# Kernel tuning notes

Hardware: AMD Instinct MI355X
Metric: run time of the kernel (lower is better)

## Reference

```python
import jax, jax.numpy as jnp
import numpy as np

B, C, N, D = 8192, 1000, 2, 512
EPS = 0.1  # epsilon init arg


def setup_inputs() -> dict:
    key = jax.random.key(0)
    kx, kc, kr = jax.random.split(key, 3)
    x = jax.random.normal(kx, (B, D), dtype=jnp.float32)
    centroids = jax.random.uniform(kc, (C, N, D), minval=-1.0, maxval=1.0, dtype=jnp.float32)
    rej_raw = jax.random.uniform(kr, (C * N, D), minval=-1.0, maxval=1.0, dtype=jnp.float32)
    # replicate the __init__ rescaling of the (frozen) rejective centroids
    cmax = jnp.max(jnp.linalg.norm(centroids, axis=-1))
    rej = 2.0 * cmax * rej_raw / (jnp.linalg.norm(rej_raw, axis=-1, keepdims=True) + 1e-16)
    return {"x": x, "centroids": centroids, "rejective_centroids": rej, "return_dists": 1}


def reference(x, centroids, rejective_centroids, return_dists):
    b, d = x.shape
    c, n, _ = centroids.shape
    t = c * n
    # centroid_norm is updated via .data in torch -> detached
    cnorm = jax.lax.stop_gradient(jnp.max(jnp.linalg.norm(centroids, axis=-1)))
    cf = (centroids / (cnorm + 1e-16)).reshape(t, d)  # [T, D] normalized centroids
    # pairwise L2 distances via the expansion identity (no [B,T,D] intermediate)
    x2 = jnp.sum(x * x, axis=-1)          # [B]
    c2 = jnp.sum(cf * cf, axis=-1)        # [T]
    d2 = jnp.maximum(x2[:, None] + c2[None, :] - 2.0 * (x @ cf.T), 0.0)
    dist = jnp.sqrt(d2)                   # [B, T]
    min_dist_class = jnp.min(dist.reshape(b, c, n), axis=2)  # [B, C]
    y = -min_dist_class
    if return_dists:
        idx = jnp.argmin(dist, axis=1)                 # [B]
        closest = cf[idx]                              # [B, D] gathered closest centroid
        r = rejective_centroids                        # [T, D]
        r2 = jnp.sum(r * r, axis=-1)                   # [T]
        xr = x @ r.T                                   # [B, T]
        cr = closest @ r.T                             # [B, T]
        cx = jnp.sum(closest * x, axis=-1)             # [B]
        cl2 = jnp.sum(closest * closest, axis=-1)      # [B]
        # w = closest - r ; b_off = -w . (closest + r)/2 = -0.5(|c|^2 - |r|^2)
        num = jnp.abs(cx[:, None] - xr - 0.5 * (cl2[:, None] - r2[None, :]))
        den = jnp.sqrt(jnp.maximum(cl2[:, None] + r2[None, :] - 2.0 * cr, 0.0)) + 1e-9
        rej_hd = jnp.min(num / den, axis=-1)           # [B]
        return jnp.concatenate([y, rej_hd[:, None]], axis=1)
    min_d = jnp.min(min_dist_class, axis=1)
    removed = jnp.where(min_dist_class == min_d[:, None], jnp.inf, min_dist_class)
    second = jnp.min(removed, axis=1)
    y_bot = -(1.0 - EPS) / (1.0 + EPS) * second
    accept = min_d - EPS * (min_d + second)
    soft = jax.nn.sigmoid(accept)  # ac_temp == 1
    return jnp.concatenate([y, y_bot[:, None], soft[:, None]], axis=1)
```

## Files before the change

### kernel.cpp

```cpp
#include <hip/hip_runtime.h>
#include <math.h>
#include <stdint.h>

#define NB   8192
#define NCLS 1000
#define NT   2000
#define ND   512
#define OUTW 1001

#define OFF_NORM2C 0
#define OFF_R2     2048
#define OFF_X2     4096
#define OFF_SCAL   12288
#define OFF_IDX    12352
#define OFF_CX     20544
#define OFF_CL2    28736

#define NOFF_MIND  36928
#define NOFF_REJP  823360

#define OFF8_MIND  36928
#define OFF8_MINT  102464
#define OFF8_MDOT  168000
#define OFF8_REJP  233536

#define PACKX_B  (8ull<<20)
#define PACKC_B  (24ull<<20)
#define PACKR_B  (28ull<<20)
#define PACKT_B  (32ull<<20)
#define WS_NEED  (48ull<<20)

typedef __attribute__((ext_vector_type(8))) short bf16x8;
typedef __attribute__((ext_vector_type(4))) float f32x4;

__global__ __launch_bounds__(64) void rownorm_kernel(
    const float* __restrict__ cen, const float* __restrict__ rej,
    const float* __restrict__ x, float* __restrict__ ws)
{
    int row = blockIdx.x;
    int lane = threadIdx.x;
    const float* src;
    int dstoff;
    if (row < NT)        { src = cen + (size_t)row * ND;          dstoff = OFF_NORM2C + row; }
    else if (row < 2*NT) { src = rej + (size_t)(row - NT) * ND;   dstoff = OFF_R2 + (row - NT); }
    else                 { src = x   + (size_t)(row - 2*NT) * ND; dstoff = OFF_X2 + (row - 2*NT); }
    float s = 0.f;
#pragma unroll
    for (int k = 0; k < ND / 64; ++k) { float v = src[lane + k * 64]; s += v * v; }
#pragma unroll
    for (int off = 32; off > 0; off >>= 1) s += __shfl_down(s, off);
    if (lane == 0) ws[dstoff] = s;
}

__global__ __launch_bounds__(256) void maxnorm_kernel(float* __restrict__ ws)
{
    __shared__ float sm[256];
    int tid = threadIdx.x;
    float m = 0.f;
    for (int i = tid; i < NT; i += 256) m = fmaxf(m, ws[OFF_NORM2C + i]);
    sm[tid] = m;
    __syncthreads();
    for (int s = 128; s > 0; s >>= 1) {
        if (tid < s) sm[tid] = fmaxf(sm[tid], sm[tid + s]);
        __syncthreads();
    }
    if (tid == 0) {
        float cnorm = sqrtf(sm[0]);
        float inv = 1.f / (cnorm + 1e-16f);
        ws[OFF_SCAL + 0] = cnorm;
        ws[OFF_SCAL + 1] = inv;
        ws[OFF_SCAL + 2] = inv * inv;
    }
}

__device__ __forceinline__ ushort bf16rn(float f){
    uint32_t u = __float_as_uint(f);
    return (ushort)((u + 0x7fffu + ((u >> 16) & 1u)) >> 16);
}

__global__ __launch_bounds__(256) void pack_kernel(const float* __restrict__ src,
    unsigned char* __restrict__ dst, int validRows)
{
    int tid = threadIdx.x;
    int lane = tid & 63;
    int W = blockIdx.x * 4 + (tid >> 6);
    int s  = W >> 4;
    int ks = W & 15;
    int row = s * 16 + (lane & 15);
    int k   = ks * 32 + (lane >> 4) * 8;
    float v[8];
    if (row < validRows) {
        float4 a = *(const float4*)&src[(size_t)row * ND + k];
        float4 b = *(const float4*)&src[(size_t)row * ND + k + 4];
        v[0]=a.x; v[1]=a.y; v[2]=a.z; v[3]=a.w;
        v[4]=b.x; v[5]=b.y; v[6]=b.z; v[7]=b.w;
    } else {
#pragma unroll
        for (int j = 0; j < 8; ++j) v[j] = 0.f;
    }
    union { ushort h[8]; uint4 q; } H, L;
#pragma unroll
    for (int j = 0; j < 8; ++j) {
        ushort hb = bf16rn(v[j]);
        float hf = __uint_as_float(((uint32_t)hb) << 16);
        H.h[j] = hb;
        L.h[j] = bf16rn(v[j] - hf);
    }
    size_t base = ((size_t)(((s >> 3) * 16 + ks) * 16 + (s & 7) * 2)) * 1024;
    *(uint4*)(dst + base + lane * 16)        = H.q;
    *(uint4*)(dst + base + 1024 + lane * 16) = L.q;
}

typedef __attribute__((address_space(3))) unsigned int lds_u32;
typedef const __attribute__((address_space(1))) unsigned int glb_u32;
__device__ __forceinline__ void gload_lds16(const unsigned char* g, unsigned char* l) {
    __builtin_amdgcn_global_load_lds((glb_u32*)g, (lds_u32*)l, 16, 0, 0);
}

template<bool BLO>
__device__ __forceinline__ void stage256(
    const unsigned char* __restrict__ aP2, const unsigned char* __restrict__ bP2,
    int ks, unsigned char* lbuf, int wave, int lane)
{
    if (wave < 4) {
#pragma unroll
        for (int j = 0; j < 8; ++j) {
            int gc = wave * 8 + j;
            gload_lds16(aP2 + (gc >> 4) * 262144 + ks * 16384 + (gc & 15) * 1024 + lane * 16,
                        lbuf + gc * 1024);
        }
    } else {
        if constexpr (BLO) {
#pragma unroll
            for (int j = 0; j < 8; ++j) {
                int gc = (wave - 4) * 8 + j;
                gload_lds16(bP2 + (gc >> 4) * 262144 + ks * 16384 + (gc & 15) * 1024 + lane * 16,
                            lbuf + 32768 + gc * 1024);
            }
        } else {
#pragma unroll
            for (int j = 0; j < 4; ++j) {
                int gc = (wave - 4) * 4 + j;
                gload_lds16(bP2 + (gc >> 3) * 262144 + ks * 16384 + ((gc & 7) * 2) * 1024 + lane * 16,
                            lbuf + 32768 + gc * 1024);
            }
        }
    }
}

#define PASS8(av, bv) do { _Pragma("unroll") \
    for (int qi = 0; qi < 4; ++qi) \
        _Pragma("unroll") \
        for (int ri = 0; ri < 8; ++ri) \
            acc[ri][qi] = __builtin_amdgcn_mfma_f32_16x16x32_bf16( \
                av[ri], bv[qi], acc[ri][qi], 0, 0, 0); \
    } while (0)

template<bool BLO>
__device__ __forceinline__ void compute_step256(
    const unsigned char* __restrict__ cbuf, int lane, int wr, int wc, f32x4 acc[8][4])
{
    const unsigned char* aB = cbuf + wr * 16384 + lane * 16;
    const unsigned char* bB = BLO
        ? cbuf + 32768 + (wc >> 1) * 16384 + ((wc & 1) * 4) * 2048 + lane * 16
        : cbuf + 32768 + (wc >> 1) * 8192  + ((wc & 1) * 4) * 1024 + lane * 16;
    bf16x8 bh[4];
#pragma unroll
    for (int qi = 0; qi < 4; ++qi) bh[qi] = *(const bf16x8*)(bB + qi * (BLO ? 2048 : 1024));
    if constexpr (BLO) {
        bf16x8 bl[4];
#pragma unroll
        for (int qi = 0; qi < 4; ++qi) bl[qi] = *(const bf16x8*)(bB + qi * 2048 + 1024);
        {
            bf16x8 a[8];
#pragma unroll
            for (int ri = 0; ri < 8; ++ri) a[ri] = *(const bf16x8*)(aB + ri * 2048);
            PASS8(a, bh);
            PASS8(a, bl);
        }
        {
            bf16x8 a[8];
#pragma unroll
            for (int ri = 0; ri < 8; ++ri) a[ri] = *(const bf16x8*)(aB + ri * 2048 + 1024);
            PASS8(a, bh);
        }
    } else {
        {
            bf16x8 a[8];
#pragma unroll
            for (int ri = 0; ri < 8; ++ri) a[ri] = *(const bf16x8*)(aB + ri * 2048);
            PASS8(a, bh);
        }
        {
            bf16x8 a[8];
#pragma unroll
            for (int ri = 0; ri < 8; ++ri) a[ri] = *(const bf16x8*)(aB + ri * 2048 + 1024);
            PASS8(a, bh);
        }
    }
}

#define SCHED_FENCE __builtin_amdgcn_sched_barrier(0)

template<bool BLO>
__device__ __forceinline__ void mfma_core256_pipe(
    const unsigned char* __restrict__ aP2, const unsigned char* __restrict__ bP2,
    unsigned char* lds, int lane, int wave, int wr, int wc, f32x4 acc[8][4])
{
    constexpr int BUF = BLO ? 65536 : 49152;
    stage256<BLO>(aP2, bP2, 0, lds, wave, lane);
    for (int ks = 0; ks < 16; ++ks) {
        unsigned char* cbuf = lds + (ks & 1) * BUF;
        unsigned char* nbuf = lds + ((ks + 1) & 1) * BUF;
        if (ks < 15) {
            stage256<BLO>(aP2, bP2, ks + 1, nbuf, wave, lane);
            SCHED_FENCE;
            if (BLO || wave < 4) asm volatile("s_waitcnt vmcnt(8)" ::: "memory");
            else                 asm volatile("s_waitcnt vmcnt(4)" ::: "memory");
            SCHED_FENCE;
        } else {
            SCHED_FENCE;
            asm volatile("s_waitcnt vmcnt(0)" ::: "memory");
            SCHED_FENCE;
        }
        __builtin_amdgcn_s_barrier();
        __builtin_amdgcn_s_setprio(1);
        compute_step256<BLO>(cbuf, lane, wr, wc, acc);
        __builtin_amdgcn_s_setprio(0);
        __builtin_amdgcn_s_barrier();
    }
}

__global__ __launch_bounds__(512) void dist_mfma_kernel(
    const unsigned char* __restrict__ xpack, const unsigned char* __restrict__ cpack,
    float* __restrict__ out, float* __restrict__ ws)
{
    __shared__ unsigned char lds[2 * 65536];
    int tid = threadIdx.x, lane = tid & 63, wave = tid >> 6;
    int wr = wave >> 2, wc = wave & 3;
    int xb = blockIdx.x, yb = blockIdx.y;
    int b0 = xb * 256, t0base = yb * 256;
    f32x4 acc[8][4];
#pragma unroll
    for (int i = 0; i < 8; ++i)
#pragma unroll
        for (int q = 0; q < 4; ++q) acc[i][q] = (f32x4){0.f, 0.f, 0.f, 0.f};
    mfma_core256_pipe<true>(xpack + (size_t)xb * 524288, cpack + (size_t)yb * 524288,
                            lds, lane, wave, wr, wc, acc);

    float inv  = ws[OFF_SCAL + 1];
    float inv2 = ws[OFF_SCAL + 2];
    int rq = lane >> 4, cidx = lane & 15;
    int seg = yb * 4 + wc;
    float c2q[4]; int tq[4];
#pragma unroll
    for (int qi = 0; qi < 4; ++qi) {
        int t = t0base + wc * 64 + qi * 16 + cidx;
        tq[qi] = t;
        c2q[qi] = (t < NT) ? ws[OFF_NORM2C + t] * inv2 : 0.f;
    }
    unsigned long long* keys = (unsigned long long*)(ws + NOFF_MIND);

#pragma unroll
    for (int ri = 0; ri < 8; ++ri) {
#pragma unroll
        for (int reg = 0; reg < 4; ++reg) {
            int row = b0 + wr * 128 + ri * 16 + rq * 4 + reg;
            float x2 = ws[OFF_X2 + row];
            unsigned long long best = ~0ull;
#pragma unroll
            for (int qi = 0; qi < 4; ++qi) {
                float dsc = acc[ri][qi][reg] * inv;
                float dd = sqrtf(fmaxf(x2 + c2q[qi] - 2.f * dsc, 0.f));
                float dn = __shfl_xor(dd, 1);
                int t = tq[qi];
                if ((t < NT) && ((cidx & 1) == 0))
                    out[(size_t)row * OUTW + (t >> 1)] = -fminf(dd, dn);
                if (t < NT) {
                    unsigned long long key =
                        ((unsigned long long)__float_as_uint(dd) << 32) | (unsigned)t;
                    best = best < key ? best : key;
                }
            }
#pragma unroll
            for (int off = 1; off < 16; off <<= 1) {
                unsigned long long o = __shfl_xor(best, off);
                best = best < o ? best : o;
            }
            if (cidx == 0) keys[(size_t)row * 32 + seg] = best;
        }
    }
}

__global__ __launch_bounds__(256) void combine32_kernel(float* __restrict__ ws)
{
    int b = blockIdx.x * 256 + threadIdx.x;
    const unsigned long long* keys = (const unsigned long long*)(ws + NOFF_MIND);
    unsigned long long best = keys[(size_t)b * 32];
#pragma unroll
    for (int s = 1; s < 32; ++s) {
        unsigned long long k = keys[(size_t)b * 32 + s];
        best = best < k ? best : k;
    }
    int bt = (int)(best & 0xffffffffull);
    float dd = __uint_as_float((unsigned)(best >> 32));
    float c2 = ws[OFF_NORM2C + bt] * ws[OFF_SCAL + 2];
    float x2 = ws[OFF_X2 + b];
    ((int*)ws)[OFF_IDX + b] = bt;
    ws[OFF_CX + b] = 0.5f * (x2 + c2 - dd * dd);
    ws[OFF_CL2 + b] = c2;
}

#define LOADA(buf, ks_) do { _Pragma("unroll") \
    for (int i = 0; i < 4; ++i) { \
        buf[i]     = *(const bf16x8*)(aB + (ks_) * 16384 + i * 2048); \
        buf[4 + i] = *(const bf16x8*)(aB + (ks_) * 16384 + i * 2048 + 1024); \
    } } while (0)
#define LOADB2(buf, ks_) do { _Pragma("unroll") \
    for (int i = 0; i < 4; ++i) { \
        buf[i] = *(const bf16x8*)(bB + (ks_) * 16384 + i * 2048); \
    } } while (0)
#define PASS(av, bv, AOFF, BOFF) do { _Pragma("unroll") \
    for (int qi = 0; qi < 4; ++qi) \
        _Pragma("unroll") \
        for (int ri = 0; ri < 4; ++ri) \
            acc[ri][qi] = __builtin_amdgcn_mfma_f32_16x16x32_bf16( \
                av[(AOFF) + ri], bv[(BOFF) + qi], acc[ri][qi], 0, 0, 0); \
    } while (0)
#define COMPUTE2(av, bv) do { PASS(av, bv, 0, 0); PASS(av, bv, 4, 0); } while (0)

__device__ __forceinline__ void mfma_core_db2(
    const unsigned char* __restrict__ aP, const unsigned char* __restrict__ bP,
    int lane, int wr, int wc, f32x4 acc[4][4])
{
    const unsigned char* aB = aP + wr * 8192 + lane * 16;
    const unsigned char* bB = bP + wc * 8192 + lane * 16;
    bf16x8 a0[8], a1[8], b0[4], b1[4];
    LOADA(a0, 0); LOADB2(b0, 0);
    for (int ks = 0; ks < 16; ks += 2) {
        LOADA(a1, ks + 1); LOADB2(b1, ks + 1);
        COMPUTE2(a0, b0);
        if (ks + 2 < 16) { LOADA(a0, ks + 2); LOADB2(b0, ks + 2); }
        COMPUTE2(a1, b1);
    }
}

__global__ __launch_bounds__(256, 2) void table_mfma_kernel(
    const unsigned char* __restrict__ cpack, const unsigned char* __restrict__ rpack,
    float* __restrict__ table, const float* __restrict__ ws)
{
    int tid = threadIdx.x, lane = tid & 63, wave = tid >> 6;
    int wr = wave >> 1, wc = wave & 1;
    int c0 = blockIdx.x * 128, t0base = blockIdx.y * 128;
    f32x4 acc[4][4];
#pragma unroll
    for (int i = 0; i < 4; ++i)
#pragma unroll
        for (int q = 0; q < 4; ++q) acc[i][q] = (f32x4){0.f, 0.f, 0.f, 0.f};
    mfma_core_db2(cpack + (size_t)blockIdx.x * 262144, rpack + (size_t)blockIdx.y * 262144,
                  lane, wr, wc, acc);

    float inv  = ws[OFF_SCAL + 1];
    float inv2 = ws[OFF_SCAL + 2];
    int rq = lane >> 4, cidx = lane & 15;
    float r2q[4]; int tq[4];
#pragma unroll
    for (int qi = 0; qi < 4; ++qi) {
        int t = t0base + wc * 64 + qi * 16 + cidx;
        tq[qi] = t;
        r2q[qi] = (t < NT) ? ws[OFF_R2 + t] : 0.f;
    }
#pragma unroll
    for (int ri = 0; ri < 4; ++ri) {
#pragma unroll
        for (int reg = 0; reg < 4; ++reg) {
            int c = c0 + wr * 64 + ri * 16 + rq * 4 + reg;
            if (c < NT) {
                float cl2c = ws[OFF_NORM2C + c] * inv2;
#pragma unroll
                for (int qi = 0; qi < 4; ++qi) {
                    int t = tq[qi];
                    if (t < NT) {
                        float cfr = acc[ri][qi][reg] * inv;
                        float den = sqrtf(fmaxf(cl2c + r2q[qi] - 2.f * cfr, 0.f)) + 1e-9f;
                        table[(size_t)c * 2048 + t] = 1.f / den;
                    }
                }
            }
        }
    }
}

__global__ __launch_bounds__(512) void xr_mfma_kernel(
    const unsigned char* __restrict__ xpack, const unsigned char* __restrict__ rpack,
    const float* __restrict__ table, float* __restrict__ ws)
{
    __shared__ unsigned char lds[2 * 49152];
    int tid = threadIdx.x, lane = tid & 63, wave = tid >> 6;
    int wr = wave >> 2, wc = wave & 3;
    int xb = blockIdx.x, yb = blockIdx.y;
    int b0 = xb * 256, t0base = yb * 256;
    f32x4 acc[8][4];
#pragma unroll
    for (int i = 0; i < 8; ++i)
#pragma unroll
        for (int q = 0; q < 4; ++q) acc[i][q] = (f32x4){0.f, 0.f, 0.f, 0.f};
    mfma_core256_pipe<false>(xpack + (size_t)xb * 524288, rpack + (size_t)yb * 524288,
                             lds, lane, wave, wr, wc, acc);

    int rq = lane >> 4, cidx = lane & 15;
    int seg = yb * 4 + wc;
    float r2q[4]; int tq[4];
#pragma unroll
    for (int qi = 0; qi < 4; ++qi) {
        int t = t0base + wc * 64 + qi * 16 + cidx;
        tq[qi] = t;
        r2q[qi] = (t < NT) ? ws[OFF_R2 + t] : 0.f;
    }
#pragma unroll
    for (int ri = 0; ri < 8; ++ri) {
#pragma unroll
        for (int reg = 0; reg < 4; ++reg) {
            int row = b0 + wr * 128 + ri * 16 + rq * 4 + reg;
            int idx = ((const int*)ws)[OFF_IDX + row];
            float cx  = ws[OFF_CX + row];
            float cl2 = ws[OFF_CL2 + row];
            const float* trow = table + (size_t)idx * 2048;
            float mv = INFINITY;
#pragma unroll
            for (int qi = 0; qi < 4; ++qi) {
                int t = tq[qi];
                if (t < NT) {
                    float num = fabsf(cx - acc[ri][qi][reg] - 0.5f * (cl2 - r2q[qi]));
                    mv = fminf(mv, num * trow[t]);
                }
            }
#pragma unroll
            for (int off = 1; off < 16; off <<= 1) mv = fminf(mv, __shfl_xor(mv, off));
            if (cidx == 0) ws[NOFF_REJP + (size_t)row * 32 + seg] = mv;
        }
    }
}

__global__ __launch_bounds__(256) void rejcombine32_kernel(
    const float* __restrict__ ws, float* __restrict__ out)
{
    int b = blockIdx.x * 256 + threadIdx.x;
    float bd = ws[NOFF_REJP + (size_t)b * 32];
#pragma unroll
    for (int s = 1; s < 32; ++s) bd = fminf(bd, ws[NOFF_REJP + (size_t)b * 32 + s]);
    out[(size_t)b * OUTW + NCLS] = bd;
}

#define BK   32
#define LDST 68

__global__ __launch_bounds__(256) void dist_kernel(
    const float* __restrict__ x, const float* __restrict__ cen,
    float* __restrict__ out, float* __restrict__ ws)
{
    __shared__ float Xs[BK][LDST];
    __shared__ float Cs[BK][LDST];
    __shared__ float red_d[64][17];
    __shared__ int   red_t[64][17];
    __shared__ float red_x[64][17];

    int tid = threadIdx.x;
    int tx = tid & 15, ty = tid >> 4;
    int b0 = blockIdx.x * 64;
    int tseg0 = blockIdx.y * 256;
    int tseg1 = min(tseg0 + 256, NT);

    float inv  = ws[OFF_SCAL + 1];
    float inv2 = ws[OFF_SCAL + 2];
    float x2v[4];
#pragma unroll
    for (int i = 0; i < 4; ++i) x2v[i] = ws[OFF_X2 + b0 + ty * 4 + i];

    int lr = tid >> 2;
    int lc = (tid & 3) * 8;

    float mind[4], mdot[4];
    int mint[4];
#pragma unroll
    for (int i = 0; i < 4; ++i) { mind[i] = INFINITY; mint[i] = 0x7fffffff; mdot[i] = 0.f; }

    for (int t0 = tseg0; t0 < tseg1; t0 += 64) {
        float acc[4][4];
#pragma unroll
        for (int i = 0; i < 4; ++i)
#pragma unroll
            for (int jj = 0; jj < 4; ++jj) acc[i][jj] = 0.f;

        for (int k0 = 0; k0 < ND; k0 += BK) {
            {
                const float4 v0 = *(const float4*)&x[(size_t)(b0 + lr) * ND + k0 + lc];
                const float4 v1 = *(const float4*)&x[(size_t)(b0 + lr) * ND + k0 + lc + 4];
                Xs[lc + 0][lr] = v0.x; Xs[lc + 1][lr] = v0.y; Xs[lc + 2][lr] = v0.z; Xs[lc + 3][lr] = v0.w;
                Xs[lc + 4][lr] = v1.x; Xs[lc + 5][lr] = v1.y; Xs[lc + 6][lr] = v1.z; Xs[lc + 7][lr] = v1.w;
            }
            {
                int tr = t0 + lr;
                float4 v0 = make_float4(0.f, 0.f, 0.f, 0.f), v1 = v0;
                if (tr < NT) {
                    v0 = *(const float4*)&cen[(size_t)tr * ND + k0 + lc];
                    v1 = *(const float4*)&cen[(size_t)tr * ND + k0 + lc + 4];
                }
                Cs[lc + 0][lr] = v0.x; Cs[lc + 1][lr] = v0.y; Cs[lc + 2][lr] = v0.z; Cs[lc + 3][lr] = v0.w;
                Cs[lc + 4][lr] = v1.x; Cs[lc + 5][lr] = v1.y; Cs[lc + 6][lr] = v1.z; Cs[lc + 7][lr] = v1.w;
            }
            __syncthreads();
#pragma unroll
            for (int kk = 0; kk < BK; ++kk) {
                float4 av = *(const float4*)&Xs[kk][ty * 4];
                float4 bv = *(const float4*)&Cs[kk][tx * 4];
                float a[4] = {av.x, av.y, av.z, av.w};
                float bb[4] = {bv.x, bv.y, bv.z, bv.w};
#pragma unroll
                for (int i = 0; i < 4; ++i)
#pragma unroll
                    for (int jj = 0; jj < 4; ++jj)
                        acc[i][jj] = fmaf(a[i], bb[jj], acc[i][jj]);
            }
            __syncthreads();
        }

        float distv[4][4];
#pragma unroll
        for (int jj = 0; jj < 4; ++jj) {
            int t = t0 + tx * 4 + jj;
            bool valid = (t < NT);
            float c2 = valid ? ws[OFF_NORM2C + t] * inv2 : 0.f;
#pragma unroll
            for (int i = 0; i < 4; ++i) {
                float dsc = acc[i][jj] * inv;
                float d2 = x2v[i] + c2 - 2.f * dsc;
                float dd = sqrtf(fmaxf(d2, 0.f));
                distv[i][jj] = dd;
                if (valid && (dd < mind[i])) { mind[i] = dd; mint[i] = t; mdot[i] = dsc; }
            }
        }
#pragma unroll
        for (int jp = 0; jp < 2; ++jp) {
            int t = t0 + tx * 4 + jp * 2;
            if (t < NT) {
                int cls = t >> 1;
#pragma unroll
                for (int i = 0; i < 4; ++i) {
                    out[(size_t)(b0 + ty * 4 + i) * OUTW + cls] =
                        -fminf(distv[i][jp * 2], distv[i][jp * 2 + 1]);
                }
            }
        }
    }

#pragma unroll
    for (int i = 0; i < 4; ++i) {
        red_d[ty * 4 + i][tx] = mind[i];
        red_t[ty * 4 + i][tx] = mint[i];
        red_x[ty * 4 + i][tx] = mdot[i];
    }
    __syncthreads();
    if (tid < 64) {
        float bd = red_d[tid][0]; int bt = red_t[tid][0]; float bx = red_x[tid][0];
        for (int q = 1; q < 16; ++q) {
            float d = red_d[tid][q]; int tt = red_t[tid][q];
            if (d < bd || (d == bd && tt < bt)) { bd = d; bt = tt; bx = red_x[tid][q]; }
        }
        int b = b0 + tid;
        int s = blockIdx.y;
        ws[OFF8_MIND + b * 8 + s] = bd;
        ((int*)ws)[OFF8_MINT + b * 8 + s] = bt;
        ws[OFF8_MDOT + b * 8 + s] = bx;
    }
}

__global__ __launch_bounds__(256) void combine_kernel(float* __restrict__ ws)
{
    int b = blockIdx.x * 256 + threadIdx.x;
    float bd = ws[OFF8_MIND + b * 8];
    int   bt = ((int*)ws)[OFF8_MINT + b * 8];
    float bx = ws[OFF8_MDOT + b * 8];
#pragma unroll
    for (int s = 1; s < 8; ++s) {
        float d = ws[OFF8_MIND + b * 8 + s];
        int  tt = ((int*)ws)[OFF8_MINT + b * 8 + s];
        if (d < bd || (d == bd && tt < bt)) { bd = d; bt = tt; bx = ws[OFF8_MDOT + b * 8 + s]; }
    }
    ((int*)ws)[OFF_IDX + b] = bt;
    ws[OFF_CX + b] = bx;
    ws[OFF_CL2 + b] = ws[OFF_NORM2C + bt] * ws[OFF_SCAL + 2];
}

__global__ __launch_bounds__(256) void rej_kernel(
    const float* __restrict__ x, const float* __restrict__ cen,
    const float* __restrict__ rej, float* __restrict__ ws)
{
    __shared__ float Xs[BK][LDST];
    __shared__ float Rs[BK][LDST];
    __shared__ float Ls[BK][LDST];
    __shared__ int idxL[64];
    __shared__ float red_d[64][17];

    int tid = threadIdx.x;
    int tx = tid & 15, ty = tid >> 4;
    int b0 = blockIdx.x * 64;
    int tseg0 = blockIdx.y * 256;
    int tseg1 = min(tseg0 + 256, NT);
    float inv = ws[OFF_SCAL + 1];

    if (tid < 64) idxL[tid] = ((int*)ws)[OFF_IDX + b0 + tid];
    float cxv[4], cl2v[4];
#pragma unroll
    for (int i = 0; i < 4; ++i) {
        cxv[i]  = ws[OFF_CX  + b0 + ty * 4 + i];
        cl2v[i] = ws[OFF_CL2 + b0 + ty * 4 + i];
    }
    __syncthreads();

    int lr = tid >> 2, lc = (tid & 3) * 8;
    int myrow = idxL[lr];

    float minv[4] = {INFINITY, INFINITY, INFINITY, INFINITY};

    for (int t0 = tseg0; t0 < tseg1; t0 += 64) {
        float xr[4][4], cr[4][4];
#pragma unroll
        for (int i = 0; i < 4; ++i)
#pragma unroll
            for (int jj = 0; jj < 4; ++jj) { xr[i][jj] = 0.f; cr[i][jj] = 0.f; }

        for (int k0 = 0; k0 < ND; k0 += BK) {
            {
                const float4 v0 = *(const float4*)&x[(size_t)(b0 + lr) * ND + k0 + lc];
                const float4 v1 = *(const float4*)&x[(size_t)(b0 + lr) * ND + k0 + lc + 4];
                Xs[lc + 0][lr] = v0.x; Xs[lc + 1][lr] = v0.y; Xs[lc + 2][lr] = v0.z; Xs[lc + 3][lr] = v0.w;
                Xs[lc + 4][lr] = v1.x; Xs[lc + 5][lr] = v1.y; Xs[lc + 6][lr] = v1.z; Xs[lc + 7][lr] = v1.w;
            }
            {
                const float4 v0 = *(const float4*)&cen[(size_t)myrow * ND + k0 + lc];
                const float4 v1 = *(const float4*)&cen[(size_t)myrow * ND + k0 + lc + 4];
                Ls[lc + 0][lr] = v0.x * inv; Ls[lc + 1][lr] = v0.y * inv;
                Ls[lc + 2][lr] = v0.z * inv; Ls[lc + 3][lr] = v0.w * inv;
                Ls[lc + 4][lr] = v1.x * inv; Ls[lc + 5][lr] = v1.y * inv;
                Ls[lc + 6][lr] = v1.z * inv; Ls[lc + 7][lr] = v1.w * inv;
            }
            {
                int tr = t0 + lr;
                float4 v0 = make_float4(0.f, 0.f, 0.f, 0.f), v1 = v0;
                if (tr < NT) {
                    v0 = *(const float4*)&rej[(size_t)tr * ND + k0 + lc];
                    v1 = *(const float4*)&rej[(size_t)tr * ND + k0 + lc + 4];
                }
                Rs[lc + 0][lr] = v0.x; Rs[lc + 1][lr] = v0.y; Rs[lc + 2][lr] = v0.z; Rs[lc + 3][lr] = v0.w;
                Rs[lc + 4][lr] = v1.x; Rs[lc + 5][lr] = v1.y; Rs[lc + 6][lr] = v1.z; Rs[lc + 7][lr] = v1.w;
            }
            __syncthreads();
#pragma unroll
            for (int kk = 0; kk < BK; ++kk) {
                float4 av = *(const float4*)&Xs[kk][ty * 4];
                float4 lv = *(const float4*)&Ls[kk][ty * 4];
                float4 rv = *(const float4*)&Rs[kk][tx * 4];
                float a[4] = {av.x, av.y, av.z, av.w};
                float l[4] = {lv.x, lv.y, lv.z, lv.w};
                float r[4] = {rv.x, rv.y, rv.z, rv.w};
#pragma unroll
                for (int i = 0; i < 4; ++i)
#pragma unroll
                    for (int jj = 0; jj < 4; ++jj) {
                        xr[i][jj] = fmaf(a[i], r[jj], xr[i][jj]);
                        cr[i][jj] = fmaf(l[i], r[jj], cr[i][jj]);
                    }
            }
            __syncthreads();
        }

#pragma unroll
        for (int jj = 0; jj < 4; ++jj) {
            int t = t0 + tx * 4 + jj;
            if (t < NT) {
                float r2 = ws[OFF_R2 + t];
#pragma unroll
                for (int i = 0; i < 4; ++i) {
                    float num = fabsf(cxv[i] - xr[i][jj] - 0.5f * (cl2v[i] - r2));
                    float den = sqrtf(fmaxf(cl2v[i] + r2 - 2.f * cr[i][jj], 0.f)) + 1e-9f;
                    minv[i] = fminf(minv[i], num / den);
                }
            }
        }
    }

#pragma unroll
    for (int i = 0; i < 4; ++i) red_d[ty * 4 + i][tx] = minv[i];
    __syncthreads();
    if (tid < 64) {
        float bd = red_d[tid][0];
        for (int q = 1; q < 16; ++q) bd = fminf(bd, red_d[tid][q]);
        ws[OFF8_REJP + (size_t)(b0 + tid) * 8 + blockIdx.y] = bd;
    }
}

__global__ __launch_bounds__(256) void rejcombine_kernel(
    const float* __restrict__ ws, float* __restrict__ out)
{
    int b = blockIdx.x * 256 + threadIdx.x;
    float bd = ws[OFF8_REJP + b * 8];
#pragma unroll
    for (int s = 1; s < 8; ++s) bd = fminf(bd, ws[OFF8_REJP + b * 8 + s]);
    out[(size_t)b * OUTW + NCLS] = bd;
}

extern "C" void kernel_launch(void* const* d_in, const int* in_sizes, int n_in,
                              void* d_out, int out_size, void* d_ws, size_t ws_size,
                              hipStream_t stream)
{
    const float* x   = (const float*)d_in[0];
    const float* cen = (const float*)d_in[1];
    const float* rej = (const float*)d_in[2];
    float* out = (float*)d_out;
    float* ws  = (float*)d_ws;
    unsigned char* wsb = (unsigned char*)d_ws;

    rownorm_kernel<<<2 * NT + NB, 64, 0, stream>>>(cen, rej, x, ws);
    maxnorm_kernel<<<1, 256, 0, stream>>>(ws);

    if (ws_size >= WS_NEED) {
        pack_kernel<<<2048, 256, 0, stream>>>(x,   wsb + PACKX_B, NB);
        pack_kernel<<<512,  256, 0, stream>>>(cen, wsb + PACKC_B, NT);
        pack_kernel<<<512,  256, 0, stream>>>(rej, wsb + PACKR_B, NT);
        dist_mfma_kernel<<<dim3(32, 8), 512, 0, stream>>>(wsb + PACKX_B, wsb + PACKC_B, out, ws);
        combine32_kernel<<<32, 256, 0, stream>>>(ws);
        table_mfma_kernel<<<dim3(16, 16), 256, 0, stream>>>(wsb + PACKC_B, wsb + PACKR_B,
                                                            (float*)(wsb + PACKT_B), ws);
        xr_mfma_kernel<<<dim3(32, 8), 512, 0, stream>>>(wsb + PACKX_B, wsb + PACKR_B,
                                                        (float*)(wsb + PACKT_B), ws);
        rejcombine32_kernel<<<32, 256, 0, stream>>>(ws, out);
    } else {
        dist_kernel<<<dim3(NB / 64, 8), 256, 0, stream>>>(x, cen, out, ws);
        combine_kernel<<<NB / 256, 256, 0, stream>>>(ws);
        rej_kernel<<<dim3(NB / 64, 8), 256, 0, stream>>>(x, cen, rej, ws);
        rejcombine_kernel<<<NB / 256, 256, 0, stream>>>(ws, out);
    }
}
```

Measured before the change: 185.5 us.

## Split 256x256 MFMA tiles across 16 waves with smaller per-wave accumulators

The distance and x·r MFMA kernels now launch 1024 threads (16 waves) per block instead of 512. Each wave computes a 64x64 sub-tile with a 4x4 accumulator array instead of 128x64 with 8x4, and staging is redistributed so every wave issues fewer async global-to-LDS loads. The aim is to cut register pressure and add waves for latency hiding, at the cost of more LDS fragment reads per MFMA and heavier barrier synchronisation. The dist epilogue also moves sqrt after the pair-min and keys the argmin on squared distance, dropping a sqrt per element and a square in the combine step.

```diff
diff --git a/kernel.cpp b/kernel.cpp
--- a/kernel.cpp
+++ b/kernel.cpp
@@ -118,105 +118,87 @@
 }
 
 template<bool BLO>
-__device__ __forceinline__ void stage256(
+__device__ __forceinline__ void stage64(
     const unsigned char* __restrict__ aP2, const unsigned char* __restrict__ bP2,
     int ks, unsigned char* lbuf, int wave, int lane)
 {
-    if (wave < 4) {
-#pragma unroll
-        for (int j = 0; j < 8; ++j) {
-            int gc = wave * 8 + j;
-            gload_lds16(aP2 + (gc >> 4) * 262144 + ks * 16384 + (gc & 15) * 1024 + lane * 16,
+    if (wave < 8) {
+#pragma unroll
+        for (int j = 0; j < 4; ++j) {
+            int gc = wave * 4 + j, s = gc >> 1, pl = gc & 1;
+            gload_lds16(aP2 + ((s >> 3) * 16 + ks) * 16384 + ((s & 7) * 2 + pl) * 1024 + lane * 16,
                         lbuf + gc * 1024);
         }
+    } else if constexpr (BLO) {
+#pragma unroll
+        for (int j = 0; j < 4; ++j) {
+            int gc = (wave - 8) * 4 + j, s = gc >> 1, pl = gc & 1;
+            gload_lds16(bP2 + ((s >> 3) * 16 + ks) * 16384 + ((s & 7) * 2 + pl) * 1024 + lane * 16,
+                        lbuf + 32768 + gc * 1024);
+        }
     } else {
-        if constexpr (BLO) {
-#pragma unroll
-            for (int j = 0; j < 8; ++j) {
-                int gc = (wave - 4) * 8 + j;
-                gload_lds16(bP2 + (gc >> 4) * 262144 + ks * 16384 + (gc & 15) * 1024 + lane * 16,
-                            lbuf + 32768 + gc * 1024);
-            }
-        } else {
-#pragma unroll
-            for (int j = 0; j < 4; ++j) {
-                int gc = (wave - 4) * 4 + j;
-                gload_lds16(bP2 + (gc >> 3) * 262144 + ks * 16384 + ((gc & 7) * 2) * 1024 + lane * 16,
-                            lbuf + 32768 + gc * 1024);
-            }
-        }
-    }
-}
-
-#define PASS8(av, bv) do { _Pragma("unroll") \
+#pragma unroll
+        for (int j = 0; j < 2; ++j) {
+            int cs = (wave - 8) * 2 + j;
+            gload_lds16(bP2 + ((cs >> 3) * 16 + ks) * 16384 + ((cs & 7) * 2) * 1024 + lane * 16,
+                        lbuf + 32768 + cs * 1024);
+        }
+    }
+}
+
+#define PASS4(av, bv) do { _Pragma("unroll") \
     for (int qi = 0; qi < 4; ++qi) \
         _Pragma("unroll") \
-        for (int ri = 0; ri < 8; ++ri) \
+        for (int ri = 0; ri < 4; ++ri) \
             acc[ri][qi] = __builtin_amdgcn_mfma_f32_16x16x32_bf16( \
                 av[ri], bv[qi], acc[ri][qi], 0, 0, 0); \
     } while (0)
 
 template<bool BLO>
-__device__ __forceinline__ void compute_step256(
-    const unsigned char* __restrict__ cbuf, int lane, int wr, int wc, f32x4 acc[8][4])
-{
-    const unsigned char* aB = cbuf + wr * 16384 + lane * 16;
-    const unsigned char* bB = BLO
-        ? cbuf + 32768 + (wc >> 1) * 16384 + ((wc & 1) * 4) * 2048 + lane * 16
-        : cbuf + 32768 + (wc >> 1) * 8192  + ((wc & 1) * 4) * 1024 + lane * 16;
-    bf16x8 bh[4];
-#pragma unroll
-    for (int qi = 0; qi < 4; ++qi) bh[qi] = *(const bf16x8*)(bB + qi * (BLO ? 2048 : 1024));
+__device__ __forceinline__ void compute_step64(
+    const unsigned char* __restrict__ cbuf, int lane, int wr, int wc, f32x4 acc[4][4])
+{
+    const unsigned char* aB = cbuf + wr * 8192 + lane * 16;
+    const unsigned char* bB = BLO ? cbuf + 32768 + wc * 8192 + lane * 16
+                                  : cbuf + 32768 + wc * 4096 + lane * 16;
+    bf16x8 ah[4], bh[4];
+#pragma unroll
+    for (int i = 0; i < 4; ++i) {
+        ah[i] = *(const bf16x8*)(aB + i * 2048);
+        bh[i] = *(const bf16x8*)(bB + i * (BLO ? 2048 : 1024));
+    }
+    PASS4(ah, bh);
     if constexpr (BLO) {
         bf16x8 bl[4];
 #pragma unroll
-        for (int qi = 0; qi < 4; ++qi) bl[qi] = *(const bf16x8*)(bB + qi * 2048 + 1024);
-        {
-            bf16x8 a[8];
-#pragma unroll
-            for (int ri = 0; ri < 8; ++ri) a[ri] = *(const bf16x8*)(aB + ri * 2048);
-            PASS8(a, bh);
-            PASS8(a, bl);
-        }
-        {
-            bf16x8 a[8];
-#pragma unroll
-            for (int ri = 0; ri < 8; ++ri) a[ri] = *(const bf16x8*)(aB + ri * 2048 + 1024);
-            PASS8(a, bh);
-        }
-    } else {
-        {
-            bf16x8 a[8];
-#pragma unroll
-            for (int ri = 0; ri < 8; ++ri) a[ri] = *(const bf16x8*)(aB + ri * 2048);
-            PASS8(a, bh);
-        }
-        {
-            bf16x8 a[8];
-#pragma unroll
-            for (int ri = 0; ri < 8; ++ri) a[ri] = *(const bf16x8*)(aB + ri * 2048 + 1024);
-            PASS8(a, bh);
-        }
+        for (int i = 0; i < 4; ++i) bl[i] = *(const bf16x8*)(bB + i * 2048 + 1024);
+        PASS4(ah, bl);
+    }
+    {
+        bf16x8 al[4];
+#pragma unroll
+        for (int i = 0; i < 4; ++i) al[i] = *(const bf16x8*)(aB + i * 2048 + 1024);
+        PASS4(al, bh);
     }
 }
 
 #define SCHED_FENCE __builtin_amdgcn_sched_barrier(0)
 
 template<bool BLO>
-__device__ __forceinline__ void mfma_core256_pipe(
+__device__ __forceinline__ void mfma_core64_pipe(
     const unsigned char* __restrict__ aP2, const unsigned char* __restrict__ bP2,
-    unsigned char* lds, int lane, int wave, int wr, int wc, f32x4 acc[8][4])
+    unsigned char* lds, int lane, int wave, int wr, int wc, f32x4 acc[4][4])
 {
     constexpr int BUF = BLO ? 65536 : 49152;
-    stage256<BLO>(aP2, bP2, 0, lds, wave, lane);
+    stage64<BLO>(aP2, bP2, 0, lds, wave, lane);
     for (int ks = 0; ks < 16; ++ks) {
         unsigned char* cbuf = lds + (ks & 1) * BUF;
         unsigned char* nbuf = lds + ((ks + 1) & 1) * BUF;
         if (ks < 15) {
-            stage256<BLO>(aP2, bP2, ks + 1, nbuf, wave, lane);
+            stage64<BLO>(aP2, bP2, ks + 1, nbuf, wave, lane);
             SCHED_FENCE;
-            if (BLO || wave < 4) asm volatile("s_waitcnt vmcnt(8)" ::: "memory");
-            else                 asm volatile("s_waitcnt vmcnt(4)" ::: "memory");
+            if (BLO || wave < 8) asm volatile("s_waitcnt vmcnt(4)" ::: "memory");
+            else                 asm volatile("s_waitcnt vmcnt(2)" ::: "memory");
             SCHED_FENCE;
         } else {
             SCHED_FENCE;
@@ -225,13 +207,13 @@
         }
         __builtin_amdgcn_s_barrier();
         __builtin_amdgcn_s_setprio(1);
-        compute_step256<BLO>(cbuf, lane, wr, wc, acc);
+        compute_step64<BLO>(cbuf, lane, wr, wc, acc);
         __builtin_amdgcn_s_setprio(0);
         __builtin_amdgcn_s_barrier();
     }
 }
 
-__global__ __launch_bounds__(512) void dist_mfma_kernel(
+__global__ __launch_bounds__(1024) void dist_mfma_kernel(
     const unsigned char* __restrict__ xpack, const unsigned char* __restrict__ cpack,
     float* __restrict__ out, float* __restrict__ ws)
 {
@@ -240,13 +222,13 @@
     int wr = wave >> 2, wc = wave & 3;
     int xb = blockIdx.x, yb = blockIdx.y;
     int b0 = xb * 256, t0base = yb * 256;
-    f32x4 acc[8][4];
-#pragma unroll
-    for (int i = 0; i < 8; ++i)
+    f32x4 acc[4][4];
+#pragma unroll
+    for (int i = 0; i < 4; ++i)
 #pragma unroll
         for (int q = 0; q < 4; ++q) acc[i][q] = (f32x4){0.f, 0.f, 0.f, 0.f};
-    mfma_core256_pipe<true>(xpack + (size_t)xb * 524288, cpack + (size_t)yb * 524288,
-                            lds, lane, wave, wr, wc, acc);
+    mfma_core64_pipe<true>(xpack + (size_t)xb * 524288, cpack + (size_t)yb * 524288,
+                           lds, lane, wave, wr, wc, acc);
 
     float inv  = ws[OFF_SCAL + 1];
     float inv2 = ws[OFF_SCAL + 2];
@@ -262,23 +244,22 @@
     unsigned long long* keys = (unsigned long long*)(ws + NOFF_MIND);
 
 #pragma unroll
-    for (int ri = 0; ri < 8; ++ri) {
+    for (int ri = 0; ri < 4; ++ri) {
 #pragma unroll
         for (int reg = 0; reg < 4; ++reg) {
-            int row = b0 + wr * 128 + ri * 16 + rq * 4 + reg;
+            int row = b0 + wr * 64 + ri * 16 + rq * 4 + reg;
             float x2 = ws[OFF_X2 + row];
             unsigned long long best = ~0ull;
 #pragma unroll
             for (int qi = 0; qi < 4; ++qi) {
-                float dsc = acc[ri][qi][reg] * inv;
-                float dd = sqrtf(fmaxf(x2 + c2q[qi] - 2.f * dsc, 0.f));
-                float dn = __shfl_xor(dd, 1);
+                float d2 = fmaxf(x2 + c2q[qi] - 2.f * (acc[ri][qi][reg] * inv), 0.f);
+                float d2n = __shfl_xor(d2, 1);
                 int t = tq[qi];
                 if ((t < NT) && ((cidx & 1) == 0))
-                    out[(size_t)row * OUTW + (t >> 1)] = -fminf(dd, dn);
+                    out[(size_t)row * OUTW + (t >> 1)] = -sqrtf(fminf(d2, d2n));
                 if (t < NT) {
                     unsigned long long key =
-                        ((unsigned long long)__float_as_uint(dd) << 32) | (unsigned)t;
+                        ((unsigned long long)__float_as_uint(d2) << 32) | (unsigned)t;
                     best = best < key ? best : key;
                 }
             }
@@ -303,11 +284,11 @@
         best = best < k ? best : k;
     }
     int bt = (int)(best & 0xffffffffull);
-    float dd = __uint_as_float((unsigned)(best >> 32));
+    float d2 = __uint_as_float((unsigned)(best >> 32));
     float c2 = ws[OFF_NORM2C + bt] * ws[OFF_SCAL + 2];
     float x2 = ws[OFF_X2 + b];
     ((int*)ws)[OFF_IDX + b] = bt;
-    ws[OFF_CX + b] = 0.5f * (x2 + c2 - dd * dd);
+    ws[OFF_CX + b] = 0.5f * (x2 + c2 - d2);
     ws[OFF_CL2 + b] = c2;
 }
 
@@ -391,7 +372,7 @@
     }
 }
 
-__global__ __launch_bounds__(512) void xr_mfma_kernel(
+__global__ __launch_bounds__(1024) void xr_mfma_kernel(
     const unsigned char* __restrict__ xpack, const unsigned char* __restrict__ rpack,
     const float* __restrict__ table, float* __restrict__ ws)
 {
@@ -400,13 +381,13 @@
     int wr = wave >> 2, wc = wave & 3;
     int xb = blockIdx.x, yb = blockIdx.y;
     int b0 = xb * 256, t0base = yb * 256;
-    f32x4 acc[8][4];
-#pragma unroll
-    for (int i = 0; i < 8; ++i)
+    f32x4 acc[4][4];
+#pragma unroll
+    for (int i = 0; i < 4; ++i)
 #pragma unroll
         for (int q = 0; q < 4; ++q) acc[i][q] = (f32x4){0.f, 0.f, 0.f, 0.f};
-    mfma_core256_pipe<false>(xpack + (size_t)xb * 524288, rpack + (size_t)yb * 524288,
-                             lds, lane, wave, wr, wc, acc);
+    mfma_core64_pipe<false>(xpack + (size_t)xb * 524288, rpack + (size_t)yb * 524288,
+                            lds, lane, wave, wr, wc, acc);
 
     int rq = lane >> 4, cidx = lane & 15;
     int seg = yb * 4 + wc;
@@ -418,10 +399,10 @@
         r2q[qi] = (t < NT) ? ws[OFF_R2 + t] : 0.f;
     }
 #pragma unroll
-    for (int ri = 0; ri < 8; ++ri) {
+    for (int ri = 0; ri < 4; ++ri) {
 #pragma unroll
         for (int reg = 0; reg < 4; ++reg) {
-            int row = b0 + wr * 128 + ri * 16 + rq * 4 + reg;
+            int row = b0 + wr * 64 + ri * 16 + rq * 4 + reg;
             int idx = ((const int*)ws)[OFF_IDX + row];
             float cx  = ws[OFF_CX + row];
             float cl2 = ws[OFF_CL2 + row];
@@ -728,12 +709,12 @@
         pack_kernel<<<2048, 256, 0, stream>>>(x,   wsb + PACKX_B, NB);
         pack_kernel<<<512,  256, 0, stream>>>(cen, wsb + PACKC_B, NT);
         pack_kernel<<<512,  256, 0, stream>>>(rej, wsb + PACKR_B, NT);
-        dist_mfma_kernel<<<dim3(32, 8), 512, 0, stream>>>(wsb + PACKX_B, wsb + PACKC_B, out, ws);
+        dist_mfma_kernel<<<dim3(32, 8), 1024, 0, stream>>>(wsb + PACKX_B, wsb + PACKC_B, out, ws);
         combine32_kernel<<<32, 256, 0, stream>>>(ws);
         table_mfma_kernel<<<dim3(16, 16), 256, 0, stream>>>(wsb + PACKC_B, wsb + PACKR_B,
                                                             (float*)(wsb + PACKT_B), ws);
-        xr_mfma_kernel<<<dim3(32, 8), 512, 0, stream>>>(wsb + PACKX_B, wsb + PACKR_B,
-                                                        (float*)(wsb + PACKT_B), ws);
+        xr_mfma_kernel<<<dim3(32, 8), 1024, 0, stream>>>(wsb + PACKX_B, wsb + PACKR_B,
+                                                         (float*)(wsb + PACKT_B), ws);
         rejcombine32_kernel<<<32, 256, 0, stream>>>(ws, out);
     } else {
         dist_kernel<<<dim3(NB / 64, 8), 256, 0, stream>>>(x, cen, out, ws);
```

New measurement: 161.4 us. -13.0%, faster.
